# Optimization experiments

Hardware: AMD Instinct MI355X
Metric: run time of the kernel (lower is better)

Reference implementation:

```python
import jax, jax.numpy as jnp
import numpy as np

BC = 256      # block_channel
RC = 64       # reduced_channel = BC // 4
NB0, NB1 = 4, 3   # num_blocks per modality (1024/256, 768/256)
TB = NB0 + NB1    # total_blocks
EPS = 1e-5        # BatchNorm eps (eval mode, running_mean=0, running_var=1)
LOWEST = 0.0      # lowest_atten


def setup_inputs() -> dict:
    key = jax.random.key(0)
    k = jax.random.split(key, 4)
    B, T = 8, 4096
    x0 = jax.random.normal(k[0], (B, 1024, T), jnp.float32)
    x1 = jax.random.normal(k[1], (B, 768, T), jnp.float32)
    W1 = jax.random.normal(k[2], (BC, RC), jnp.float32) / np.sqrt(BC).astype(np.float32)
    b1 = jnp.zeros((RC,), jnp.float32)
    gamma = jnp.ones((RC,), jnp.float32)
    beta = jnp.zeros((RC,), jnp.float32)
    Wh = jax.random.normal(k[3], (TB, RC, BC), jnp.float32) / np.sqrt(RC).astype(np.float32)
    bh = jnp.zeros((TB, BC), jnp.float32)
    return {"x0": x0, "x1": x1, "W1": W1, "b1": b1, "gamma": gamma,
            "beta": beta, "Wh": Wh, "bh": bh}


def reference(x0, x1, W1, b1, gamma, beta, Wh, bh):
    B, _, T = x0.shape
    # split channels into blocks: [B, nb, BC, T]
    xr0 = x0.reshape(B, NB0, BC, T)
    xr1 = x1.reshape(B, NB1, BC, T)
    # block-sum over blocks, then global average pool over time -> [B, BC]
    gap = xr0.sum(axis=1).mean(axis=-1) + xr1.sum(axis=1).mean(axis=-1)
    # joint projector: Linear -> BatchNorm1d(eval: mean=0, var=1) -> ReLU
    h = gap @ W1 + b1
    h = jnp.maximum(h * (gamma / jnp.sqrt(1.0 + EPS)) + beta, 0.0)  # [B, RC]
    # all TB attention heads as one grouped GEMM: [TB, B, BC]
    scores = jnp.einsum('br,krc->kbc', h, Wh) + bh[:, None, :]
    att = jax.nn.softmax(scores, axis=0)          # softmax over block axis (dim=0)
    att = jnp.transpose(att, (1, 0, 2))           # [B, TB, BC]
    att = LOWEST + att * (1.0 - LOWEST)
    # scale each block's features
    out0 = (xr0 * att[:, :NB0, :, None]).reshape(x0.shape)
    out1 = (xr1 * att[:, NB0:, :, None]).reshape(x1.shape)
    return (out0, out1)
```

## Files before the change

kernel.cpp:

```cpp
#include <hip/hip_runtime.h>

#define B_SZ 8
#define T_SZ 4096
#define BC 256
#define RC 64
#define NB0 4
#define NB1 3
#define TB 7
#define ROWS0 (B_SZ * 1024)
#define ROWS1 (B_SZ * 768)
#define ROWS_TOTAL (ROWS0 + ROWS1)
#define X0_ELEMS (33554432ull)

typedef float vfloat4 __attribute__((ext_vector_type(4)));

__global__ __launch_bounds__(256) void rowsum_kernel(const float* __restrict__ x0,
                                                     const float* __restrict__ x1,
                                                     float* __restrict__ rowsum) {
    const int gtid = blockIdx.x * 256 + threadIdx.x;
    const int wave = gtid >> 6;
    const int lane = threadIdx.x & 63;

    const float4* src = (wave < ROWS0)
        ? (const float4*)(x0 + (size_t)wave * T_SZ)
        : (const float4*)(x1 + (size_t)(wave - ROWS0) * T_SZ);

    float sum = 0.0f;
#pragma unroll
    for (int it = 0; it < 16; ++it) {
        float4 v = src[it * 64 + lane];
        sum += (v.x + v.y) + (v.z + v.w);
    }
#pragma unroll
    for (int off = 32; off > 0; off >>= 1)
        sum += __shfl_down(sum, off, 64);

    if (lane == 0)
        rowsum[wave] = sum;
}

__global__ __launch_bounds__(256) void att_kernel(const float* __restrict__ rowsum,
                                                  const float* __restrict__ W1,
                                                  const float* __restrict__ b1,
                                                  const float* __restrict__ gamma,
                                                  const float* __restrict__ beta,
                                                  const float* __restrict__ Wh,
                                                  const float* __restrict__ bh,
                                                  float* __restrict__ att) {
    __shared__ float s_gap[BC];
    __shared__ float s_h[RC];
    const int tid = threadIdx.x;
    const int b = blockIdx.x;

    float s = 0.0f;
#pragma unroll
    for (int blk = 0; blk < NB0; ++blk)
        s += rowsum[b * 1024 + blk * 256 + tid];
#pragma unroll
    for (int blk = 0; blk < NB1; ++blk)
        s += rowsum[ROWS0 + b * 768 + blk * 256 + tid];
    s_gap[tid] = s * (1.0f / (float)T_SZ);
    __syncthreads();

    if (tid < RC) {
        const float bnscale = rsqrtf(1.0f + 1e-5f);
        float acc = 0.0f;
#pragma unroll 8
        for (int c = 0; c < BC; ++c)
            acc = fmaf(s_gap[c], W1[c * RC + tid], acc);
        acc += b1[tid];
        acc = acc * (gamma[tid] * bnscale) + beta[tid];
        s_h[tid] = fmaxf(acc, 0.0f);
    }
    __syncthreads();

    float sc[TB];
#pragma unroll
    for (int k = 0; k < TB; ++k)
        sc[k] = bh[k * BC + tid];
    for (int r = 0; r < RC; ++r) {
        const float hr = s_h[r];
#pragma unroll
        for (int k = 0; k < TB; ++k)
            sc[k] = fmaf(Wh[(k * RC + r) * BC + tid], hr, sc[k]);
    }
    float mx = -1e30f;
#pragma unroll
    for (int k = 0; k < TB; ++k) mx = fmaxf(mx, sc[k]);
    float sum = 0.0f;
#pragma unroll
    for (int k = 0; k < TB; ++k) { sc[k] = __expf(sc[k] - mx); sum += sc[k]; }
    const float inv = 1.0f / sum;
#pragma unroll
    for (int k = 0; k < TB; ++k)
        att[(b * TB + k) * BC + tid] = sc[k] * inv;
}

__global__ __launch_bounds__(256) void scale_kernel(const float* __restrict__ x0,
                                                    const float* __restrict__ x1,
                                                    const float* __restrict__ att,
                                                    float* __restrict__ out) {
    const int row = blockIdx.x * 4 + (threadIdx.x >> 6);
    const int lane = threadIdx.x & 63;

    const vfloat4* src;
    vfloat4* dst;
    float a;
    if (row < ROWS0) {
        const int b = row >> 10;
        const int ch = row & 1023;
        a = att[(b * TB + (ch >> 8)) * BC + (ch & 255)];
        src = (const vfloat4*)(x0 + (size_t)row * T_SZ);
        dst = (vfloat4*)(out + (size_t)row * T_SZ);
    } else {
        const int r = row - ROWS0;
        const int b = (int)((unsigned)r / 768u);
        const int ch = r - b * 768;
        a = att[(b * TB + NB0 + (ch >> 8)) * BC + (ch & 255)];
        src = (const vfloat4*)(x1 + (size_t)r * T_SZ);
        dst = (vfloat4*)(out + X0_ELEMS + (size_t)r * T_SZ);
    }

#pragma unroll
    for (int it = 0; it < 16; ++it) {
        vfloat4 v = __builtin_nontemporal_load(&src[it * 64 + lane]);
        v *= a;
        __builtin_nontemporal_store(v, &dst[it * 64 + lane]);
    }
}

extern "C" void kernel_launch(void* const* d_in, const int* in_sizes, int n_in,
                              void* d_out, int out_size, void* d_ws, size_t ws_size,
                              hipStream_t stream) {
    const float* x0    = (const float*)d_in[0];
    const float* x1    = (const float*)d_in[1];
    const float* W1    = (const float*)d_in[2];
    const float* b1    = (const float*)d_in[3];
    const float* gamma = (const float*)d_in[4];
    const float* beta  = (const float*)d_in[5];
    const float* Wh    = (const float*)d_in[6];
    const float* bh    = (const float*)d_in[7];
    float* out = (float*)d_out;

    float* rowsum = out;
    float* att = (float*)d_ws;

    rowsum_kernel<<<ROWS_TOTAL / 4, 256, 0, stream>>>(x0, x1, rowsum);
    att_kernel<<<B_SZ, 256, 0, stream>>>(rowsum, W1, b1, gamma, beta, Wh, bh, att);
    scale_kernel<<<ROWS_TOTAL / 4, 256, 0, stream>>>(x0, x1, att, out);
}
```

Measured before the change: 449.1 us.

## Fuse rowsum, attention and scale into one cooperative persistent kernel

Replaces the three-kernel sequence with a single cooperative kernel that runs the row-sum phase, a grid sync, the per-batch attention computation, another grid sync, and the scaling phase, using grid-stride loops over rows. The goal is to remove the launch gaps and tail effects between kernels. In exchange it adds two grid-wide barriers, and only eight blocks do the attention step while the rest of the grid waits. Grid size comes from the occupancy query and is capped, and the old three-kernel path remains as a fallback.

```diff
diff --git a/kernel.cpp b/kernel.cpp
--- a/kernel.cpp
+++ b/kernel.cpp
@@ -1,4 +1,7 @@
 #include <hip/hip_runtime.h>
+#include <hip/hip_cooperative_groups.h>
+
+namespace cg = cooperative_groups;
 
 #define B_SZ 8
 #define T_SZ 4096
@@ -11,8 +14,122 @@
 #define ROWS1 (B_SZ * 768)
 #define ROWS_TOTAL (ROWS0 + ROWS1)
 #define X0_ELEMS (33554432ull)
+#define MAX_COOP_BLOCKS 1792
 
 typedef float vfloat4 __attribute__((ext_vector_type(4)));
+
+__global__ __launch_bounds__(256, 4) void fused_kernel(const float* __restrict__ x0,
+                                                       const float* __restrict__ x1,
+                                                       const float* __restrict__ W1,
+                                                       const float* __restrict__ b1,
+                                                       const float* __restrict__ gamma,
+                                                       const float* __restrict__ beta,
+                                                       const float* __restrict__ Wh,
+                                                       const float* __restrict__ bh,
+                                                       float* __restrict__ out,
+                                                       float* __restrict__ att) {
+    __shared__ float s_gap[BC];
+    __shared__ float s_h[RC];
+
+    const int tid    = threadIdx.x;
+    const int lane   = tid & 63;
+    const int nwaves = gridDim.x * 4;
+    const int wid0   = blockIdx.x * 4 + (tid >> 6);
+    float* rowsum = out;
+
+    for (int row = wid0; row < ROWS_TOTAL; row += nwaves) {
+        const float4* src = (row < ROWS0)
+            ? (const float4*)(x0 + (size_t)row * T_SZ)
+            : (const float4*)(x1 + (size_t)(row - ROWS0) * T_SZ);
+        float sum = 0.0f;
+#pragma unroll
+        for (int it = 0; it < 16; ++it) {
+            float4 v = src[it * 64 + lane];
+            sum += (v.x + v.y) + (v.z + v.w);
+        }
+#pragma unroll
+        for (int off = 32; off > 0; off >>= 1)
+            sum += __shfl_down(sum, off, 64);
+        if (lane == 0)
+            rowsum[row] = sum;
+    }
+
+    cg::this_grid().sync();
+
+    if (blockIdx.x < B_SZ) {
+        const int b = blockIdx.x;
+        float s = 0.0f;
+#pragma unroll
+        for (int blk = 0; blk < NB0; ++blk)
+            s += rowsum[b * 1024 + blk * 256 + tid];
+#pragma unroll
+        for (int blk = 0; blk < NB1; ++blk)
+            s += rowsum[ROWS0 + b * 768 + blk * 256 + tid];
+        s_gap[tid] = s * (1.0f / (float)T_SZ);
+        __syncthreads();
+
+        if (tid < RC) {
+            const float bnscale = rsqrtf(1.0f + 1e-5f);
+            float acc = 0.0f;
+#pragma unroll 8
+            for (int c = 0; c < BC; ++c)
+                acc = fmaf(s_gap[c], W1[c * RC + tid], acc);
+            acc += b1[tid];
+            acc = acc * (gamma[tid] * bnscale) + beta[tid];
+            s_h[tid] = fmaxf(acc, 0.0f);
+        }
+        __syncthreads();
+
+        float sc[TB];
+#pragma unroll
+        for (int k = 0; k < TB; ++k)
+            sc[k] = bh[k * BC + tid];
+        for (int r = 0; r < RC; ++r) {
+            const float hr = s_h[r];
+#pragma unroll
+            for (int k = 0; k < TB; ++k)
+                sc[k] = fmaf(Wh[(k * RC + r) * BC + tid], hr, sc[k]);
+        }
+        float mx = -1e30f;
+#pragma unroll
+        for (int k = 0; k < TB; ++k) mx = fmaxf(mx, sc[k]);
+        float sum = 0.0f;
+#pragma unroll
+        for (int k = 0; k < TB; ++k) { sc[k] = __expf(sc[k] - mx); sum += sc[k]; }
+        const float inv = 1.0f / sum;
+#pragma unroll
+        for (int k = 0; k < TB; ++k)
+            att[(b * TB + k) * BC + tid] = sc[k] * inv;
+    }
+
+    cg::this_grid().sync();
+
+    for (int row = wid0; row < ROWS_TOTAL; row += nwaves) {
+        const vfloat4* src;
+        vfloat4* dst;
+        float a;
+        if (row < ROWS0) {
+            const int b = row >> 10;
+            const int ch = row & 1023;
+            a = att[(b * TB + (ch >> 8)) * BC + (ch & 255)];
+            src = (const vfloat4*)(x0 + (size_t)row * T_SZ);
+            dst = (vfloat4*)(out + (size_t)row * T_SZ);
+        } else {
+            const int r = row - ROWS0;
+            const int b = (int)((unsigned)r / 768u);
+            const int ch = r - b * 768;
+            a = att[(b * TB + NB0 + (ch >> 8)) * BC + (ch & 255)];
+            src = (const vfloat4*)(x1 + (size_t)r * T_SZ);
+            dst = (vfloat4*)(out + X0_ELEMS + (size_t)r * T_SZ);
+        }
+#pragma unroll
+        for (int it = 0; it < 16; ++it) {
+            vfloat4 v = __builtin_nontemporal_load(&src[it * 64 + lane]);
+            v *= a;
+            __builtin_nontemporal_store(v, &dst[it * 64 + lane]);
+        }
+    }
+}
 
 __global__ __launch_bounds__(256) void rowsum_kernel(const float* __restrict__ x0,
                                                      const float* __restrict__ x1,
@@ -20,11 +137,9 @@
     const int gtid = blockIdx.x * 256 + threadIdx.x;
     const int wave = gtid >> 6;
     const int lane = threadIdx.x & 63;
-
     const float4* src = (wave < ROWS0)
         ? (const float4*)(x0 + (size_t)wave * T_SZ)
         : (const float4*)(x1 + (size_t)(wave - ROWS0) * T_SZ);
-
     float sum = 0.0f;
 #pragma unroll
     for (int it = 0; it < 16; ++it) {
@@ -34,7 +149,6 @@
 #pragma unroll
     for (int off = 32; off > 0; off >>= 1)
         sum += __shfl_down(sum, off, 64);
-
     if (lane == 0)
         rowsum[wave] = sum;
 }
@@ -51,7 +165,6 @@
     __shared__ float s_h[RC];
     const int tid = threadIdx.x;
     const int b = blockIdx.x;
-
     float s = 0.0f;
 #pragma unroll
     for (int blk = 0; blk < NB0; ++blk)
@@ -61,7 +174,6 @@
         s += rowsum[ROWS0 + b * 768 + blk * 256 + tid];
     s_gap[tid] = s * (1.0f / (float)T_SZ);
     __syncthreads();
-
     if (tid < RC) {
         const float bnscale = rsqrtf(1.0f + 1e-5f);
         float acc = 0.0f;
@@ -73,7 +185,6 @@
         s_h[tid] = fmaxf(acc, 0.0f);
     }
     __syncthreads();
-
     float sc[TB];
 #pragma unroll
     for (int k = 0; k < TB; ++k)
@@ -102,7 +213,6 @@
                                                     float* __restrict__ out) {
     const int row = blockIdx.x * 4 + (threadIdx.x >> 6);
     const int lane = threadIdx.x & 63;
-
     const vfloat4* src;
     vfloat4* dst;
     float a;
@@ -120,7 +230,6 @@
         src = (const vfloat4*)(x1 + (size_t)r * T_SZ);
         dst = (vfloat4*)(out + X0_ELEMS + (size_t)r * T_SZ);
     }
-
 #pragma unroll
     for (int it = 0; it < 16; ++it) {
         vfloat4 v = __builtin_nontemporal_load(&src[it * 64 + lane]);
@@ -141,10 +250,37 @@
     const float* Wh    = (const float*)d_in[6];
     const float* bh    = (const float*)d_in[7];
     float* out = (float*)d_out;
+    float* att = (float*)d_ws;
+
+    static int coop_blocks = -1;
+    if (coop_blocks < 0) {
+        int per_cu = 0, n_cu = 0, dev = 0;
+        hipError_t e0 = hipGetDevice(&dev);
+        hipError_t e1 = hipOccupancyMaxActiveBlocksPerMultiprocessor(
+                            &per_cu, (const void*)fused_kernel, 256, 0);
+        hipError_t e2 = hipDeviceGetAttribute(
+                            &n_cu, hipDeviceAttributeMultiprocessorCount, dev);
+        if (e0 == hipSuccess && e1 == hipSuccess && e2 == hipSuccess &&
+            per_cu > 0 && n_cu > 0) {
+            long total = (long)per_cu * (long)n_cu;
+            coop_blocks = (int)(total > MAX_COOP_BLOCKS ? MAX_COOP_BLOCKS : total);
+        } else {
+            coop_blocks = 0;
+        }
+    }
+
+    if (coop_blocks >= B_SZ) {
+        void* args[] = {(void*)&x0, (void*)&x1, (void*)&W1, (void*)&b1,
+                        (void*)&gamma, (void*)&beta, (void*)&Wh, (void*)&bh,
+                        (void*)&out, (void*)&att};
+        hipError_t err = hipLaunchCooperativeKernel((const void*)fused_kernel,
+                                                    dim3(coop_blocks), dim3(256),
+                                                    args, 0, stream);
+        if (err == hipSuccess)
+            return;
+    }
 
     float* rowsum = out;
-    float* att = (float*)d_ws;
-
     rowsum_kernel<<<ROWS_TOTAL / 4, 256, 0, stream>>>(x0, x1, rowsum);
     att_kernel<<<B_SZ, 256, 0, stream>>>(rowsum, W1, b1, gamma, beta, Wh, bh, att);
     scale_kernel<<<ROWS_TOTAL / 4, 256, 0, stream>>>(x0, x1, att, out);
```

Result: slower. 614.2 us (+36.8%).
